# Optimization experiments

Measured on AMD Instinct MI355X. Metric: run time of the kernel, lower is better.

Reference implementation:

```python
import jax, jax.numpy as jnp
import numpy as np

NEG_SLOPE = 0.2  # PyG GATConv default negative_slope


def _gat_layer(x, src, dst, W, a_s, a_d, b, heads, ch):
    N = x.shape[0]
    h = (x @ W).reshape(N, heads, ch)                      # [N,H,C]
    al_s = jnp.sum(h * a_s[None], axis=-1)                 # [N,H]
    al_d = jnp.sum(h * a_d[None], axis=-1)                 # [N,H]
    e = jax.nn.leaky_relu(al_s[src] + al_d[dst], NEG_SLOPE)  # [E,H]
    m = jax.ops.segment_max(e, dst, num_segments=N)        # segment-softmax (stable)
    ex = jnp.exp(e - jax.lax.stop_gradient(m)[dst])
    denom = jax.ops.segment_sum(ex, dst, num_segments=N)
    alpha = ex / (denom[dst] + 1e-16)                      # [E,H]
    msg = h[src] * alpha[..., None]                        # [E,H,C]
    out = jax.ops.segment_sum(msg, dst, num_segments=N)    # [N,H,C]
    return out.reshape(N, heads * ch) + b


def _add_self_loops(edge_index, N):
    loop = jnp.arange(N, dtype=edge_index.dtype)
    src = jnp.concatenate([edge_index[0], loop])
    dst = jnp.concatenate([edge_index[1], loop])
    return src, dst


def gat_forward(x, edge_index, batch, W1, a_src1, a_dst1, b1, W2, a_src2, a_dst2, b2, W3, a_src3, a_dst3, b3, num_graphs=512):
    N = x.shape[0]
    src, dst = _add_self_loops(edge_index, N)
    x = jax.nn.relu(_gat_layer(x, src, dst, W1, a_src1, a_dst1, b1, 4, 64))
    x = jax.nn.relu(_gat_layer(x, src, dst, W2, a_src2, a_dst2, b2, 4, 64))
    x = _gat_layer(x, src, dst, W3, a_src3, a_dst3, b3, 1, 32)
    # global_mean_pool
    sums = jax.ops.segment_sum(x, batch, num_segments=num_graphs)
    cnt = jax.ops.segment_sum(jnp.ones((N,), x.dtype), batch, num_segments=num_graphs)
    return sums / jnp.maximum(cnt, 1.0)[:, None]


def setup_inputs() -> dict:
    key = jax.random.key(0)
    ks = jax.random.split(key, 16)
    N, E, G = 50000, 800000, 512
    IN, HID, H, OUT = 775, 64, 4, 32
    s = 0.05
    return {
        "x": jax.random.normal(ks[0], (N, IN), jnp.float32),
        "edge_index": jax.random.randint(ks[1], (2, E), 0, N, jnp.int32),
        "batch": jnp.sort(jax.random.randint(ks[2], (N,), 0, G, jnp.int32)),
        "W1": jax.random.normal(ks[3], (IN, H * HID), jnp.float32) * s,
        "a_src1": jax.random.normal(ks[4], (H, HID), jnp.float32) * s,
        "a_dst1": jax.random.normal(ks[5], (H, HID), jnp.float32) * s,
        "b1": jnp.zeros((H * HID,), jnp.float32),
        "W2": jax.random.normal(ks[6], (H * HID, H * HID), jnp.float32) * s,
        "a_src2": jax.random.normal(ks[7], (H, HID), jnp.float32) * s,
        "a_dst2": jax.random.normal(ks[8], (H, HID), jnp.float32) * s,
        "b2": jnp.zeros((H * HID,), jnp.float32),
        "W3": jax.random.normal(ks[9], (H * HID, OUT), jnp.float32) * s,
        "a_src3": jax.random.normal(ks[10], (1, OUT), jnp.float32) * s,
        "a_dst3": jax.random.normal(ks[11], (1, OUT), jnp.float32) * s,
        "b3": jnp.zeros((OUT,), jnp.float32),
    }


def reference(x, edge_index, batch, W1, a_src1, a_dst1, b1, W2, a_src2, a_dst2, b2, W3, a_src3, a_dst3, b3):
    return gat_forward(x, edge_index, batch, W1, a_src1, a_dst1, b1, W2, a_src2, a_dst2, b2, W3, a_src3, a_dst3, b3)
```

## Files before the change

kernel.cpp:

```cpp
#include <hip/hip_runtime.h>
#include <hip/hip_bf16.h>

typedef unsigned short u16;
typedef __attribute__((ext_vector_type(4))) unsigned short u16x4;
typedef __attribute__((ext_vector_type(8))) unsigned short u16x8;
typedef __attribute__((ext_vector_type(8))) short bf16x8;
typedef __attribute__((ext_vector_type(4))) float f32x4;

__device__ __forceinline__ u16 f2bs(float f) {
    union { float f; unsigned int u; } x; x.f = f;
    unsigned int r = x.u + 0x7FFFu + ((x.u >> 16) & 1u);
    return (u16)(r >> 16);
}
__device__ __forceinline__ float bs2f(u16 u) {
    union { unsigned int u; float f; } x; x.u = ((unsigned int)u) << 16; return x.f;
}
__device__ __forceinline__ float lrelu(float e) { return e >= 0.f ? e : 0.2f * e; }

__device__ __forceinline__ unsigned cvtpk(float lo, float hi) {
    unsigned r;
    asm("v_cvt_pk_bf16_f32 %0, %1, %2" : "=v"(r) : "v"(lo), "v"(hi));
    return r;
}

__device__ __forceinline__ void glds16(const void* g, void* l) {
    __builtin_amdgcn_global_load_lds(
        (const __attribute__((address_space(1))) unsigned int*)g,
        (__attribute__((address_space(3))) unsigned int*)l, 16, 0, 0);
}

__global__ void deg_kernel(const int* __restrict__ dst, int* __restrict__ deg, int E) {
    int i = blockIdx.x * 256 + threadIdx.x;
    if (i < E) atomicAdd(&deg[dst[i]], 1);
}

__global__ __launch_bounds__(1024) void scan_local(const int* __restrict__ deg,
        int* __restrict__ ptr, int* __restrict__ bsum, int N) {
    __shared__ int wsum[16];
    const int t = threadIdx.x, i = blockIdx.x * 1024 + t;
    const int lane = t & 63, w = t >> 6;
    int v = (i < N) ? deg[i] : 0;
    int x = v;
    #pragma unroll
    for (int off = 1; off < 64; off <<= 1) { int y = __shfl_up(x, off); if (lane >= off) x += y; }
    if (lane == 63) wsum[w] = x;
    __syncthreads();
    if (w == 0) {
        int s = (lane < 16) ? wsum[lane] : 0;
        #pragma unroll
        for (int off = 1; off < 16; off <<= 1) { int y = __shfl_up(s, off); if (lane >= off) s += y; }
        if (lane < 16) wsum[lane] = s;
    }
    __syncthreads();
    int incl = x + (w > 0 ? wsum[w - 1] : 0);
    if (i < N) ptr[i + 1] = incl;
    if (t == 0) bsum[blockIdx.x] = wsum[15];
}

__global__ __launch_bounds__(64) void scan_carry(int* __restrict__ bsum, int nb) {
    int t = threadIdx.x;
    int v = (t < nb) ? bsum[t] : 0;
    int x = v;
    #pragma unroll
    for (int off = 1; off < 64; off <<= 1) { int y = __shfl_up(x, off); if (t >= off) x += y; }
    if (t < nb) bsum[t] = x - v;
}

__global__ __launch_bounds__(1024) void scan_final(const int* __restrict__ deg,
        int* __restrict__ ptr, int* __restrict__ cur, const int* __restrict__ bsum, int N) {
    int i = blockIdx.x * 1024 + threadIdx.x;
    if (i == 0) ptr[0] = 0;
    if (i < N) {
        int p = ptr[i + 1] + bsum[blockIdx.x];
        ptr[i + 1] = p;
        cur[i] = p - deg[i];
    }
}

__global__ void fill_kernel(const int* __restrict__ src, const int* __restrict__ dst,
        int* __restrict__ cur, int* __restrict__ csr, int E) {
    int i = blockIdx.x * 256 + threadIdx.x;
    if (i < E) { int p = atomicAdd(&cur[dst[i]], 1); csr[p] = src[i]; }
}

__global__ void bounds_kernel(const int* __restrict__ batch, int* __restrict__ gstart,
        int N, int G) {
    int i = blockIdx.x * 256 + threadIdx.x;
    if (i > N) return;
    if (i == 0) {
        int b0 = batch[0];
        for (int g = 0; g <= b0; g++) gstart[g] = 0;
    } else if (i == N) {
        int bl = batch[N - 1];
        for (int g = bl + 1; g <= G; g++) gstart[g] = N;
    } else {
        int b = batch[i], bp = batch[i - 1];
        for (int g = bp + 1; g <= b; g++) gstart[g] = i;
    }
}

__global__ void transpose_w(const float* __restrict__ W, u16* __restrict__ Wt,
        int K, int Nn, int KT) {
    int idx = blockIdx.x * 256 + threadIdx.x;
    if (idx >= Nn * KT) return;
    int n = idx / KT, k = idx - n * KT;
    Wt[(size_t)n * KT + k] = (k < K) ? f2bs(W[(size_t)k * Nn + n]) : (u16)0;
}

__global__ __launch_bounds__(256) void tail_kernel(const float* __restrict__ x,
        float* __restrict__ xtail, int N) {
    int idx = blockIdx.x * 256 + threadIdx.x;
    if (idx >= N * 32) return;
    int n = idx >> 5, j = idx & 31;
    xtail[idx] = (768 + j < 775) ? x[(size_t)n * 775 + 768 + j] : 0.f;
}

__global__ __launch_bounds__(256) void gemm_glds_f32(
        const float* __restrict__ A, int lda, int M,
        const float* __restrict__ Atail,
        const u16* __restrict__ B, int ldb,
        u16* __restrict__ C, int ldc) {
    __shared__ float Aldsf[3][128][32];
    __shared__ u16   Blds[3][128][32];
    const int t = threadIdx.x;
    const int col0 = blockIdx.x * 128;
    const int row0 = blockIdx.y * 128;
    const int wid = t >> 6, lane = t & 63;
    const int wm = wid >> 1, wn = wid & 1;
    const int quad = lane >> 4, l16 = lane & 15;

    f32x4 acc[4][4];
    f32x4 z = {0.f, 0.f, 0.f, 0.f};
    #pragma unroll
    for (int i = 0; i < 4; i++)
        #pragma unroll
        for (int j = 0; j < 4; j++) acc[i][j] = z;

    const int trb = wid * 32 + (lane >> 2);
    const int arl = lane >> 3;
    const int asg = lane & 7;

    auto stage = [&](int buf, int kt) {
        const int k0 = kt << 5;
        #pragma unroll
        for (int c = 0; c < 2; c++) {
            const int tr = trb + c * 16;
            const int ks = ((lane & 3) ^ ((tr >> 1) & 3)) * 8;
            glds16(B + (size_t)(col0 + tr) * ldb + k0 + ks, &Blds[buf][wid * 32 + c * 16][0]);
        }
        #pragma unroll
        for (int c = 0; c < 4; c++) {
            const int rt = wid * 32 + c * 8 + arl;
            int gra = row0 + rt; if (gra > M - 1) gra = M - 1;
            const int sg = (asg ^ ((rt & 3) << 1)) * 4;
            const float* src = (kt < 24) ? (A + (size_t)gra * lda + k0 + sg)
                                         : (Atail + (size_t)gra * 32 + sg);
            glds16(src, &Aldsf[buf][wid * 32 + c * 8][0]);
        }
    };
    auto compute = [&](int buf) {
        bf16x8 af[4], bfr[4];
        #pragma unroll
        for (int it = 0; it < 4; it++) {
            const int r = wm * 64 + it * 16 + l16;
            const int go = ((2 * quad) ^ ((r & 3) << 1)) * 4;
            const f32x4 lo = *(const f32x4*)&Aldsf[buf][r][go];
            const f32x4 hi = *(const f32x4*)&Aldsf[buf][r][go + 4];
            union { unsigned u[4]; bf16x8 v; } uu;
            uu.u[0] = cvtpk(lo[0], lo[1]);
            uu.u[1] = cvtpk(lo[2], lo[3]);
            uu.u[2] = cvtpk(hi[0], hi[1]);
            uu.u[3] = cvtpk(hi[2], hi[3]);
            af[it] = uu.v;
        }
        #pragma unroll
        for (int jt = 0; jt < 4; jt++) {
            const int r = wn * 64 + jt * 16 + l16;
            bfr[jt] = *(const bf16x8*)&Blds[buf][r][(quad ^ ((r >> 1) & 3)) * 8];
        }
        #pragma unroll
        for (int it = 0; it < 4; it++)
            #pragma unroll
            for (int jt = 0; jt < 4; jt++)
                acc[it][jt] = __builtin_amdgcn_mfma_f32_16x16x32_bf16(af[it], bfr[jt], acc[it][jt], 0, 0, 0);
    };

    const int kTiles = 25;
    stage(0, 0);
    stage(1, 1);
    for (int kt = 0; kt < kTiles - 1; ++kt) {
        asm volatile("s_waitcnt vmcnt(6)" ::: "memory");
        __builtin_amdgcn_sched_barrier(0);
        __builtin_amdgcn_s_barrier();
        __builtin_amdgcn_sched_barrier(0);
        if (kt + 2 < kTiles) stage((kt + 2) % 3, kt + 2);
        compute(kt % 3);
    }
    asm volatile("s_waitcnt vmcnt(0)" ::: "memory");
    __builtin_amdgcn_sched_barrier(0);
    __builtin_amdgcn_s_barrier();
    __builtin_amdgcn_sched_barrier(0);
    compute((kTiles - 1) % 3);

    #pragma unroll
    for (int it = 0; it < 4; it++) {
        int gr0 = row0 + wm * 64 + it * 16 + quad * 4;
        #pragma unroll
        for (int jt = 0; jt < 4; jt++) {
            int gc = col0 + wn * 64 + jt * 16 + l16;
            #pragma unroll
            for (int r = 0; r < 4; r++) {
                int gr = gr0 + r;
                if (gr < M) C[(size_t)gr * ldc + gc] = f2bs(acc[it][jt][r]);
            }
        }
    }
}

__global__ __launch_bounds__(256) void gemm_glds(
        const u16* __restrict__ A, int lda, int M, int K,
        const u16* __restrict__ B, int ldb,
        u16* __restrict__ C, int ldc) {
    __shared__ u16 Alds[3][128][32];
    __shared__ u16 Blds[3][128][32];
    const int t = threadIdx.x;
    const int col0 = blockIdx.x * 128;
    const int row0 = blockIdx.y * 128;
    const int wid = t >> 6, lane = t & 63;
    const int wm = wid >> 1, wn = wid & 1;
    const int quad = lane >> 4, l16 = lane & 15;

    f32x4 acc[4][4];
    f32x4 z = {0.f, 0.f, 0.f, 0.f};
    #pragma unroll
    for (int i = 0; i < 4; i++)
        #pragma unroll
        for (int j = 0; j < 4; j++) acc[i][j] = z;

    const int trb = wid * 32 + (lane >> 2);

    auto stage = [&](int buf, int kt) {
        const int k0 = kt << 5;
        #pragma unroll
        for (int c = 0; c < 2; c++) {
            const int tr = trb + c * 16;
            const int ks = ((lane & 3) ^ ((tr >> 1) & 3)) * 8;
            int gra = row0 + tr; if (gra > M - 1) gra = M - 1;
            glds16(A + (size_t)gra * lda + k0 + ks, &Alds[buf][wid * 32 + c * 16][0]);
            glds16(B + (size_t)(col0 + tr) * ldb + k0 + ks, &Blds[buf][wid * 32 + c * 16][0]);
        }
    };
    auto compute = [&](int buf) {
        bf16x8 af[4], bfr[4];
        #pragma unroll
        for (int it = 0; it < 4; it++) {
            const int r = wm * 64 + it * 16 + l16;
            af[it] = *(const bf16x8*)&Alds[buf][r][(quad ^ ((r >> 1) & 3)) * 8];
        }
        #pragma unroll
        for (int jt = 0; jt < 4; jt++) {
            const int r = wn * 64 + jt * 16 + l16;
            bfr[jt] = *(const bf16x8*)&Blds[buf][r][(quad ^ ((r >> 1) & 3)) * 8];
        }
        #pragma unroll
        for (int it = 0; it < 4; it++)
            #pragma unroll
            for (int jt = 0; jt < 4; jt++)
                acc[it][jt] = __builtin_amdgcn_mfma_f32_16x16x32_bf16(af[it], bfr[jt], acc[it][jt], 0, 0, 0);
    };

    const int kTiles = K >> 5;
    stage(0, 0);
    stage(1, 1);
    for (int kt = 0; kt < kTiles - 1; ++kt) {
        asm volatile("s_waitcnt vmcnt(4)" ::: "memory");
        __builtin_amdgcn_sched_barrier(0);
        __builtin_amdgcn_s_barrier();
        __builtin_amdgcn_sched_barrier(0);
        if (kt + 2 < kTiles) stage((kt + 2) % 3, kt + 2);
        compute(kt % 3);
    }
    asm volatile("s_waitcnt vmcnt(0)" ::: "memory");
    __builtin_amdgcn_sched_barrier(0);
    __builtin_amdgcn_s_barrier();
    __builtin_amdgcn_sched_barrier(0);
    compute((kTiles - 1) % 3);

    #pragma unroll
    for (int it = 0; it < 4; it++) {
        int gr0 = row0 + wm * 64 + it * 16 + quad * 4;
        #pragma unroll
        for (int jt = 0; jt < 4; jt++) {
            int gc = col0 + wn * 64 + jt * 16 + l16;
            #pragma unroll
            for (int r = 0; r < 4; r++) {
                int gr = gr0 + r;
                if (gr < M) C[(size_t)gr * ldc + gc] = f2bs(acc[it][jt][r]);
            }
        }
    }
}

__global__ __launch_bounds__(256) void gemm32(
        const u16* __restrict__ A, int lda, int M, int K,
        const u16* __restrict__ B, int ldb, float* __restrict__ C) {
    __shared__ u16 Alds[128][40];
    __shared__ u16 Blds[32][40];
    const int t = threadIdx.x;
    const int row0 = blockIdx.x * 128;
    const int wid = t >> 6, lane = t & 63;
    const int quad = lane >> 4, l16 = lane & 15;
    f32x4 acc[2][2];
    f32x4 z = {0.f, 0.f, 0.f, 0.f};
    acc[0][0] = z; acc[0][1] = z; acc[1][0] = z; acc[1][1] = z;
    const int kTiles = K >> 5;
    for (int kt = 0; kt < kTiles; ++kt) {
        const int k0 = kt << 5;
        #pragma unroll
        for (int c = 0; c < 2; c++) {
            int ch = t + c * 256;
            int r = ch >> 2, cp = (ch & 3) * 8;
            int gr = row0 + r;
            u16x8 v = {0,0,0,0,0,0,0,0};
            if (gr < M) v = *(const u16x8*)(A + (size_t)gr * lda + k0 + cp);
            *(u16x8*)&Alds[r][cp] = v;
        }
        if (t < 128) {
            int r = t >> 2, cp = (t & 3) * 8;
            *(u16x8*)&Blds[r][cp] = *(const u16x8*)(B + (size_t)r * ldb + k0 + cp);
        }
        __syncthreads();
        bf16x8 af[2], bfr[2];
        #pragma unroll
        for (int it = 0; it < 2; it++) af[it] = *(const bf16x8*)&Alds[wid * 32 + it * 16 + l16][quad * 8];
        #pragma unroll
        for (int jt = 0; jt < 2; jt++) bfr[jt] = *(const bf16x8*)&Blds[jt * 16 + l16][quad * 8];
        #pragma unroll
        for (int it = 0; it < 2; it++)
            #pragma unroll
            for (int jt = 0; jt < 2; jt++)
                acc[it][jt] = __builtin_amdgcn_mfma_f32_16x16x32_bf16(af[it], bfr[jt], acc[it][jt], 0, 0, 0);
        __syncthreads();
    }
    #pragma unroll
    for (int it = 0; it < 2; it++) {
        int gr0 = row0 + wid * 32 + it * 16 + quad * 4;
        #pragma unroll
        for (int jt = 0; jt < 2; jt++) {
            int gc = jt * 16 + l16;
            #pragma unroll
            for (int r = 0; r < 4; r++) {
                int gr = gr0 + r;
                if (gr < M) C[(size_t)gr * 32 + gc] = acc[it][jt][r];
            }
        }
    }
}

__global__ __launch_bounds__(256) void al_kernel(const u16* __restrict__ h,
        const float* __restrict__ a_s, const float* __restrict__ a_d,
        float* __restrict__ als, float* __restrict__ ald, int N) {
    const int t = threadIdx.x, wid = t >> 6, lane = t & 63;
    const f32x4 as4 = *(const f32x4*)&a_s[lane * 4];
    const f32x4 ad4 = *(const f32x4*)&a_d[lane * 4];
    #pragma unroll
    for (int u = 0; u < 2; u++) {
        const int n = blockIdx.x * 8 + wid * 2 + u;
        if (n >= N) return;
        const u16x4 hv = *(const u16x4*)&h[(size_t)n * 256 + lane * 4];
        float ps = 0.f, pd = 0.f;
        #pragma unroll
        for (int c = 0; c < 4; c++) {
            const float f = bs2f(hv[c]);
            ps = fmaf(f, as4[c], ps);
            pd = fmaf(f, ad4[c], pd);
        }
        #pragma unroll
        for (int off = 8; off >= 1; off >>= 1) {
            ps += __shfl_xor(ps, off, 16);
            pd += __shfl_xor(pd, off, 16);
        }
        if ((lane & 15) == 0) {
            als[n * 4 + (lane >> 4)] = ps;
            ald[n * 4 + (lane >> 4)] = pd;
        }
    }
}

__global__ __launch_bounds__(256) void al3_kernel(const float* __restrict__ h3,
        const float* __restrict__ a_s, const float* __restrict__ a_d,
        float* __restrict__ als, float* __restrict__ ald, int N) {
    int t = threadIdx.x, wid = t >> 6, lane = t & 63;
    int c = lane & 31, half = lane >> 5;
    float as = a_s[c], ad = a_d[c];
    int n = blockIdx.x * 8 + wid * 2 + half;
    if (n >= N) return;
    float hv = h3[(size_t)n * 32 + c];
    float ps = hv * as, pd = hv * ad;
    for (int off = 16; off >= 1; off >>= 1) { ps += __shfl_down(ps, off, 32); pd += __shfl_down(pd, off, 32); }
    if (c == 0) { als[n] = ps; ald[n] = pd; }
}

__global__ __launch_bounds__(256) void agg_kernel(const u16* __restrict__ hbuf,
        const float* __restrict__ als, const float* __restrict__ ald,
        const int* __restrict__ ptr, const int* __restrict__ csr,
        const float* __restrict__ bias, u16* __restrict__ act, int N) {
    __shared__ float al_lds[4][64][4];
    __shared__ int   s_lds[4][64];
    const int t = threadIdx.x, wid = t >> 6, lane = t & 63;
    const int i = blockIdx.x * 4 + wid;
    if (i >= N) return;
    const int start = ptr[i], end = ptr[i + 1];
    const int deg = end - start;
    const int col8 = lane & 31;
    const int half = lane >> 5;
    const int head8 = col8 >> 3;

    const f32x4 aldv = *(const f32x4*)&ald[(size_t)i * 4];
    const f32x4 alsv = *(const f32x4*)&als[(size_t)i * 4];
    f32x4 eself;
    #pragma unroll
    for (int hh = 0; hh < 4; hh++) eself[hh] = lrelu(alsv[hh] + aldv[hh]);

    float acc[8];
    f32x4 mx, inv;

    if (deg <= 64) {
        int sreg = 0;
        f32x4 ev;
        #pragma unroll
        for (int hh = 0; hh < 4; hh++) ev[hh] = -1e30f;
        if (lane < deg) {
            sreg = csr[start + lane];
            const f32x4 a = *(const f32x4*)&als[(size_t)sreg * 4];
            #pragma unroll
            for (int hh = 0; hh < 4; hh++) ev[hh] = lrelu(a[hh] + aldv[hh]);
        }
        #pragma unroll
        for (int hh = 0; hh < 4; hh++) mx[hh] = fmaxf(eself[hh], ev[hh]);
        #pragma unroll
        for (int off = 32; off >= 1; off >>= 1) {
            #pragma unroll
            for (int hh = 0; hh < 4; hh++) mx[hh] = fmaxf(mx[hh], __shfl_xor(mx[hh], off));
        }
        f32x4 sm, av;
        #pragma unroll
        for (int hh = 0; hh < 4; hh++) {
            av[hh] = (lane < deg) ? expf(ev[hh] - mx[hh]) : 0.f;
            sm[hh] = av[hh] + ((lane == 0) ? expf(eself[hh] - mx[hh]) : 0.f);
        }
        #pragma unroll
        for (int off = 32; off >= 1; off >>= 1) {
            #pragma unroll
            for (int hh = 0; hh < 4; hh++) sm[hh] += __shfl_xor(sm[hh], off);
        }
        #pragma unroll
        for (int hh = 0; hh < 4; hh++) inv[hh] = 1.f / (sm[hh] + 1e-16f);
        #pragma unroll
        for (int hh = 0; hh < 4; hh++) av[hh] *= inv[hh];
        *(f32x4*)&al_lds[wid][lane][0] = av;
        s_lds[wid][lane] = sreg;

        const u16x8 hrs = *(const u16x8*)&hbuf[(size_t)i * 256 + col8 * 8];
        const float aself = expf(eself[head8] - mx[head8]) * inv[head8];
        #pragma unroll
        for (int c = 0; c < 8; c++) acc[c] = (half == 0) ? aself * bs2f(hrs[c]) : 0.f;

        int k = half;
        for (; k + 6 < deg; k += 8) {
            const int s0 = s_lds[wid][k],     s1 = s_lds[wid][k + 2];
            const int s2 = s_lds[wid][k + 4], s3 = s_lds[wid][k + 6];
            const float a0 = al_lds[wid][k][head8],     a1 = al_lds[wid][k + 2][head8];
            const float a2 = al_lds[wid][k + 4][head8], a3 = al_lds[wid][k + 6][head8];
            const u16x8 h0 = *(const u16x8*)&hbuf[(size_t)s0 * 256 + col8 * 8];
            const u16x8 h1 = *(const u16x8*)&hbuf[(size_t)s1 * 256 + col8 * 8];
            const u16x8 h2 = *(const u16x8*)&hbuf[(size_t)s2 * 256 + col8 * 8];
            const u16x8 h3v = *(const u16x8*)&hbuf[(size_t)s3 * 256 + col8 * 8];
            #pragma unroll
            for (int c = 0; c < 8; c++) {
                acc[c] = fmaf(a0, bs2f(h0[c]), acc[c]);
                acc[c] = fmaf(a1, bs2f(h1[c]), acc[c]);
                acc[c] = fmaf(a2, bs2f(h2[c]), acc[c]);
                acc[c] = fmaf(a3, bs2f(h3v[c]), acc[c]);
            }
        }
        for (; k < deg; k += 2) {
            const int s = s_lds[wid][k];
            const float a = al_lds[wid][k][head8];
            const u16x8 hr = *(const u16x8*)&hbuf[(size_t)s * 256 + col8 * 8];
            #pragma unroll
            for (int c = 0; c < 8; c++) acc[c] = fmaf(a, bs2f(hr[c]), acc[c]);
        }
    } else {
        mx = eself;
        for (int j = start + lane; j < end; j += 64) {
            int s = csr[j];
            const f32x4 a = *(const f32x4*)&als[(size_t)s * 4];
            #pragma unroll
            for (int hh = 0; hh < 4; hh++) mx[hh] = fmaxf(mx[hh], lrelu(a[hh] + aldv[hh]));
        }
        #pragma unroll
        for (int off = 32; off >= 1; off >>= 1) {
            #pragma unroll
            for (int hh = 0; hh < 4; hh++) mx[hh] = fmaxf(mx[hh], __shfl_xor(mx[hh], off));
        }
        f32x4 sm;
        #pragma unroll
        for (int hh = 0; hh < 4; hh++) sm[hh] = (lane == 0) ? expf(eself[hh] - mx[hh]) : 0.f;
        for (int j = start + lane; j < end; j += 64) {
            int s = csr[j];
            const f32x4 a = *(const f32x4*)&als[(size_t)s * 4];
            #pragma unroll
            for (int hh = 0; hh < 4; hh++) sm[hh] += expf(lrelu(a[hh] + aldv[hh]) - mx[hh]);
        }
        #pragma unroll
        for (int off = 32; off >= 1; off >>= 1) {
            #pragma unroll
            for (int hh = 0; hh < 4; hh++) sm[hh] += __shfl_xor(sm[hh], off);
        }
        #pragma unroll
        for (int hh = 0; hh < 4; hh++) inv[hh] = 1.f / (sm[hh] + 1e-16f);

        const u16x8 hrs = *(const u16x8*)&hbuf[(size_t)i * 256 + col8 * 8];
        const float aself = expf(eself[head8] - mx[head8]) * inv[head8];
        #pragma unroll
        for (int c = 0; c < 8; c++) acc[c] = (half == 0) ? aself * bs2f(hrs[c]) : 0.f;

        for (int base = start; base < end; base += 64) {
            const int n64 = min(64, end - base);
            const int j = base + lane;
            int sreg = 0;
            if (j < end) {
                sreg = csr[j];
                const f32x4 a = *(const f32x4*)&als[(size_t)sreg * 4];
                f32x4 alpha;
                #pragma unroll
                for (int hh = 0; hh < 4; hh++)
                    alpha[hh] = expf(lrelu(a[hh] + aldv[hh]) - mx[hh]) * inv[hh];
                *(f32x4*)&al_lds[wid][lane][0] = alpha;
            }
            s_lds[wid][lane] = sreg;
            for (int k = half; k < n64; k += 2) {
                const int s = s_lds[wid][k];
                const float a = al_lds[wid][k][head8];
                const u16x8 hr = *(const u16x8*)&hbuf[(size_t)s * 256 + col8 * 8];
                #pragma unroll
                for (int c = 0; c < 8; c++) acc[c] = fmaf(a, bs2f(hr[c]), acc[c]);
            }
        }
    }

    #pragma unroll
    for (int c = 0; c < 8; c++) acc[c] += __shfl_down(acc[c], 32);
    if (half == 0) {
        const f32x4 bv0 = *(const f32x4*)&bias[col8 * 8];
        const f32x4 bv1 = *(const f32x4*)&bias[col8 * 8 + 4];
        u16x8 o;
        #pragma unroll
        for (int c = 0; c < 4; c++) o[c] = f2bs(fmaxf(acc[c] + bv0[c], 0.f));
        #pragma unroll
        for (int c = 4; c < 8; c++) o[c] = f2bs(fmaxf(acc[c] + bv1[c - 4], 0.f));
        *(u16x8*)&act[(size_t)i * 256 + col8 * 8] = o;
    }
}

__global__ __launch_bounds__(256) void agg3_kernel(const float* __restrict__ h3,
        const float* __restrict__ als, const float* __restrict__ ald,
        const int* __restrict__ ptr, const int* __restrict__ csr,
        const float* __restrict__ bias, float* __restrict__ out_n, int N) {
    __shared__ float a_lds[4][64];
    __shared__ int   s_lds3[4][64];
    const int t = threadIdx.x, wid = t >> 6, lane = t & 63;
    const int col = lane & 31, half = lane >> 5;
    const int i = blockIdx.x * 4 + wid;
    if (i >= N) return;
    const int start = ptr[i], end = ptr[i + 1];
    const int deg = end - start;
    const float aldv = ald[i];
    const float e0 = lrelu(als[i] + aldv);
    float acc = 0.f;

    if (deg <= 64) {
        int sreg = 0; float ev = -1e30f;
        if (lane < deg) { sreg = csr[start + lane]; ev = lrelu(als[sreg] + aldv); }
        float mx = fmaxf(e0, ev);
        #pragma unroll
        for (int off = 32; off >= 1; off >>= 1) mx = fmaxf(mx, __shfl_xor(mx, off));
        float ex = (lane < deg) ? expf(ev - mx) : 0.f;
        float sm = ex + ((lane == 0) ? expf(e0 - mx) : 0.f);
        #pragma unroll
        for (int off = 32; off >= 1; off >>= 1) sm += __shfl_xor(sm, off);
        const float inv = 1.f / (sm + 1e-16f);
        a_lds[wid][lane] = ex * inv;
        s_lds3[wid][lane] = sreg;
        if (half == 0) acc = expf(e0 - mx) * inv * h3[(size_t)i * 32 + col];

        int k = half;
        for (; k + 6 < deg; k += 8) {
            const int s0 = s_lds3[wid][k],     s1 = s_lds3[wid][k + 2];
            const int s2 = s_lds3[wid][k + 4], s3 = s_lds3[wid][k + 6];
            const float a0 = a_lds[wid][k],     a1 = a_lds[wid][k + 2];
            const float a2 = a_lds[wid][k + 4], a3 = a_lds[wid][k + 6];
            const float v0 = h3[(size_t)s0 * 32 + col];
            const float v1 = h3[(size_t)s1 * 32 + col];
            const float v2 = h3[(size_t)s2 * 32 + col];
            const float v3 = h3[(size_t)s3 * 32 + col];
            acc = fmaf(a0, v0, acc); acc = fmaf(a1, v1, acc);
            acc = fmaf(a2, v2, acc); acc = fmaf(a3, v3, acc);
        }
        for (; k < deg; k += 2)
            acc = fmaf(a_lds[wid][k], h3[(size_t)s_lds3[wid][k] * 32 + col], acc);
    } else {
        float mx = e0;
        for (int j = start + lane; j < end; j += 64)
            mx = fmaxf(mx, lrelu(als[csr[j]] + aldv));
        #pragma unroll
        for (int off = 32; off >= 1; off >>= 1) mx = fmaxf(mx, __shfl_xor(mx, off));
        float sm = (lane == 0) ? expf(e0 - mx) : 0.f;
        for (int j = start + lane; j < end; j += 64)
            sm += expf(lrelu(als[csr[j]] + aldv) - mx);
        #pragma unroll
        for (int off = 32; off >= 1; off >>= 1) sm += __shfl_xor(sm, off);
        const float inv = 1.f / (sm + 1e-16f);
        if (half == 0) acc = expf(e0 - mx) * inv * h3[(size_t)i * 32 + col];
        for (int base = start; base < end; base += 64) {
            const int n64 = min(64, end - base);
            const int j = base + lane;
            int sreg = 0; float av = 0.f;
            if (j < end) {
                sreg = csr[j];
                av = expf(lrelu(als[sreg] + aldv) - mx) * inv;
            }
            a_lds[wid][lane] = av;
            s_lds3[wid][lane] = sreg;
            for (int k = half; k < n64; k += 2)
                acc = fmaf(a_lds[wid][k], h3[(size_t)s_lds3[wid][k] * 32 + col], acc);
        }
    }

    acc += __shfl_down(acc, 32);
    if (half == 0)
        out_n[(size_t)i * 32 + col] = acc + bias[col];
}

__global__ __launch_bounds__(256) void pool_kernel(const float* __restrict__ out_n,
        const int* __restrict__ gstart, float* __restrict__ out, int G) {
    const int t = threadIdx.x, wid = t >> 6, lane = t & 63;
    const int col = lane & 31, half = lane >> 5;
    const int g = blockIdx.x * 4 + wid;
    if (g >= G) return;
    const int s = gstart[g], e = gstart[g + 1];
    float acc = 0.f;
    int r = s + half;
    for (; r + 6 < e; r += 8) {
        acc += out_n[(size_t)r * 32 + col];
        acc += out_n[(size_t)(r + 2) * 32 + col];
        acc += out_n[(size_t)(r + 4) * 32 + col];
        acc += out_n[(size_t)(r + 6) * 32 + col];
    }
    for (; r < e; r += 2) acc += out_n[(size_t)r * 32 + col];
    acc += __shfl_down(acc, 32);
    if (half == 0)
        out[g * 32 + col] = acc / fmaxf((float)(e - s), 1.f);
}

extern "C" void kernel_launch(void* const* d_in, const int* in_sizes, int n_in,
                              void* d_out, int out_size, void* d_ws, size_t ws_size,
                              hipStream_t stream) {
    const int N = 50000, E = 800000, G = 512;
    const float* x    = (const float*)d_in[0];
    const int*   ei   = (const int*)d_in[1];
    const int*   batch= (const int*)d_in[2];
    const float* W1   = (const float*)d_in[3];
    const float* as1  = (const float*)d_in[4];
    const float* ad1  = (const float*)d_in[5];
    const float* b1   = (const float*)d_in[6];
    const float* W2   = (const float*)d_in[7];
    const float* as2  = (const float*)d_in[8];
    const float* ad2  = (const float*)d_in[9];
    const float* b2   = (const float*)d_in[10];
    const float* W3   = (const float*)d_in[11];
    const float* as3  = (const float*)d_in[12];
    const float* ad3  = (const float*)d_in[13];
    const float* b3   = (const float*)d_in[14];
    const int* esrc = ei;
    const int* edst = ei + E;

    char* base = (char*)d_ws; size_t off = 0;
    auto alloc = [&](size_t bytes) -> void* {
        void* p = base + off; off = (off + bytes + 255) & ~(size_t)255; return p;
    };
    u16*   hbuf = (u16*)  alloc((size_t)N * 256 * 2);
    u16*   act  = (u16*)  alloc((size_t)N * 256 * 2);
    float* h3   = (float*)alloc((size_t)N * 32 * 4);
    float* als  = (float*)alloc((size_t)N * 4 * 4);
    float* ald  = (float*)alloc((size_t)N * 4 * 4);
    int*   deg  = (int*)  alloc((size_t)N * 4);
    int*   ptr  = (int*)  alloc((size_t)(N + 1) * 4);
    int*   cur  = (int*)  alloc((size_t)N * 4);
    int*   csr  = (int*)  alloc((size_t)E * 4);
    u16*   Wt   = (u16*)  alloc((size_t)256 * 800 * 2);
    int*   bsum = (int*)  alloc((size_t)64 * 4);
    float* out_n= (float*)alloc((size_t)N * 32 * 4);
    int*   gstart=(int*)  alloc((size_t)(G + 1) * 4);
    float* xtail= (float*)alloc((size_t)N * 32 * 4);

    hipMemsetAsync(deg, 0, (size_t)N * 4, stream);

    const int nb = (N + 1023) / 1024;
    deg_kernel<<<(E + 255) / 256, 256, 0, stream>>>(edst, deg, E);
    scan_local<<<nb, 1024, 0, stream>>>(deg, ptr, bsum, N);
    scan_carry<<<1, 64, 0, stream>>>(bsum, nb);
    scan_final<<<nb, 1024, 0, stream>>>(deg, ptr, cur, bsum, N);
    fill_kernel<<<(E + 255) / 256, 256, 0, stream>>>(esrc, edst, cur, csr, E);
    bounds_kernel<<<(N + 256) / 256, 256, 0, stream>>>(batch, gstart, N, G);

    dim3 gemmGrid(2, (N + 127) / 128);
    const int aggGrid = (N + 3) / 4;
    transpose_w<<<(256 * 800 + 255) / 256, 256, 0, stream>>>(W1, Wt, 775, 256, 800);
    tail_kernel<<<(N * 32 + 255) / 256, 256, 0, stream>>>(x, xtail, N);
    gemm_glds_f32<<<gemmGrid, 256, 0, stream>>>(x, 775, N, xtail, Wt, 800, hbuf, 256);
    al_kernel<<<(N + 7) / 8, 256, 0, stream>>>(hbuf, as1, ad1, als, ald, N);
    agg_kernel<<<aggGrid, 256, 0, stream>>>(hbuf, als, ald, ptr, csr, b1, act, N);
    transpose_w<<<(256 * 256 + 255) / 256, 256, 0, stream>>>(W2, Wt, 256, 256, 256);
    gemm_glds<<<gemmGrid, 256, 0, stream>>>(act, 256, N, 256, Wt, 256, hbuf, 256);
    al_kernel<<<(N + 7) / 8, 256, 0, stream>>>(hbuf, as2, ad2, als, ald, N);
    agg_kernel<<<aggGrid, 256, 0, stream>>>(hbuf, als, ald, ptr, csr, b2, act, N);
    transpose_w<<<(32 * 256 + 255) / 256, 256, 0, stream>>>(W3, Wt, 256, 32, 256);
    gemm32<<<(N + 127) / 128, 256, 0, stream>>>(act, 256, N, 256, Wt, 256, h3);
    al3_kernel<<<(N + 7) / 8, 256, 0, stream>>>(h3, as3, ad3, als, ald, N);
    agg3_kernel<<<aggGrid, 256, 0, stream>>>(h3, als, ald, ptr, csr, b3, out_n, N);
    pool_kernel<<<(G + 3) / 4, 256, 0, stream>>>(out_n, gstart, (float*)d_out, G);
}
```

Before: 617.3 us.

## Fuse attention logit computation into GEMM epilogues and swizzle blocks across XCDs

The per-node source and destination attention logits for layers 1 and 2 are now computed in the GEMM epilogue from the bf16-rounded accumulators, using a 16-lane shuffle reduction per head. This removes the separate al_kernel launches and their re-read of the hidden buffer. The GEMM grid is flattened to 1D and remapped so that consecutive tiles land on the same XCD, which is meant to improve L2 reuse. The MFMA block is also wrapped in s_setprio raises. The epilogue now loops rows in the outer position, which changes its store pattern and adds shuffle work inside the GEMM.

```diff
diff --git a/kernel.cpp b/kernel.cpp
--- a/kernel.cpp
+++ b/kernel.cpp
@@ -27,6 +27,13 @@
     __builtin_amdgcn_global_load_lds(
         (const __attribute__((address_space(1))) unsigned int*)g,
         (__attribute__((address_space(3))) unsigned int*)l, 16, 0, 0);
+}
+
+__device__ __forceinline__ int xcd_swz(int bid, int nwg) {
+    int q = nwg >> 3, r = nwg & 7;
+    int xcd = bid & 7, pos = bid >> 3;
+    int base = (xcd < r) ? xcd * (q + 1) : r * (q + 1) + (xcd - r) * q;
+    return base + pos;
 }
 
 __global__ void deg_kernel(const int* __restrict__ dst, int* __restrict__ deg, int E) {
@@ -119,12 +126,16 @@
         const float* __restrict__ A, int lda, int M,
         const float* __restrict__ Atail,
         const u16* __restrict__ B, int ldb,
-        u16* __restrict__ C, int ldc) {
+        u16* __restrict__ C, int ldc,
+        const float* __restrict__ a_s, const float* __restrict__ a_d,
+        float* __restrict__ als, float* __restrict__ ald) {
     __shared__ float Aldsf[3][128][32];
     __shared__ u16   Blds[3][128][32];
     const int t = threadIdx.x;
-    const int col0 = blockIdx.x * 128;
-    const int row0 = blockIdx.y * 128;
+    const int id = xcd_swz(blockIdx.x, gridDim.x);
+    const int cx = id & 1;
+    const int col0 = cx * 128;
+    const int row0 = (id >> 1) * 128;
     const int wid = t >> 6, lane = t & 63;
     const int wm = wid >> 1, wn = wid & 1;
     const int quad = lane >> 4, l16 = lane & 15;
@@ -178,11 +189,13 @@
             const int r = wn * 64 + jt * 16 + l16;
             bfr[jt] = *(const bf16x8*)&Blds[buf][r][(quad ^ ((r >> 1) & 3)) * 8];
         }
+        __builtin_amdgcn_s_setprio(1);
         #pragma unroll
         for (int it = 0; it < 4; it++)
             #pragma unroll
             for (int jt = 0; jt < 4; jt++)
                 acc[it][jt] = __builtin_amdgcn_mfma_f32_16x16x32_bf16(af[it], bfr[jt], acc[it][jt], 0, 0, 0);
+        __builtin_amdgcn_s_setprio(0);
     };
 
     const int kTiles = 25;
@@ -202,16 +215,42 @@
     __builtin_amdgcn_sched_barrier(0);
     compute((kTiles - 1) % 3);
 
+    const int hd = cx * 2 + wn;
+    float asv[4], adv[4];
+    #pragma unroll
+    for (int jt = 0; jt < 4; jt++) {
+        asv[jt] = a_s[hd * 64 + jt * 16 + l16];
+        adv[jt] = a_d[hd * 64 + jt * 16 + l16];
+    }
     #pragma unroll
     for (int it = 0; it < 4; it++) {
         int gr0 = row0 + wm * 64 + it * 16 + quad * 4;
         #pragma unroll
-        for (int jt = 0; jt < 4; jt++) {
-            int gc = col0 + wn * 64 + jt * 16 + l16;
-            #pragma unroll
-            for (int r = 0; r < 4; r++) {
-                int gr = gr0 + r;
-                if (gr < M) C[(size_t)gr * ldc + gc] = f2bs(acc[it][jt][r]);
+        for (int r = 0; r < 4; r++) {
+            int gr = gr0 + r;
+            u16 ov[4];
+            float ps = 0.f, pd = 0.f;
+            #pragma unroll
+            for (int jt = 0; jt < 4; jt++) {
+                u16 o = f2bs(acc[it][jt][r]);
+                ov[jt] = o;
+                float hv = bs2f(o);
+                ps = fmaf(hv, asv[jt], ps);
+                pd = fmaf(hv, adv[jt], pd);
+            }
+            if (gr < M) {
+                #pragma unroll
+                for (int jt = 0; jt < 4; jt++)
+                    C[(size_t)gr * ldc + col0 + wn * 64 + jt * 16 + l16] = ov[jt];
+            }
+            #pragma unroll
+            for (int off = 8; off >= 1; off >>= 1) {
+                ps += __shfl_xor(ps, off, 16);
+                pd += __shfl_xor(pd, off, 16);
+            }
+            if (l16 == 0 && gr < M) {
+                als[gr * 4 + hd] = ps;
+                ald[gr * 4 + hd] = pd;
             }
         }
     }
@@ -220,12 +259,16 @@
 __global__ __launch_bounds__(256) void gemm_glds(
         const u16* __restrict__ A, int lda, int M, int K,
         const u16* __restrict__ B, int ldb,
-        u16* __restrict__ C, int ldc) {
+        u16* __restrict__ C, int ldc,
+        const float* __restrict__ a_s, const float* __restrict__ a_d,
+        float* __restrict__ als, float* __restrict__ ald) {
     __shared__ u16 Alds[3][128][32];
     __shared__ u16 Blds[3][128][32];
     const int t = threadIdx.x;
-    const int col0 = blockIdx.x * 128;
-    const int row0 = blockIdx.y * 128;
+    const int id = xcd_swz(blockIdx.x, gridDim.x);
+    const int cx = id & 1;
+    const int col0 = cx * 128;
+    const int row0 = (id >> 1) * 128;
     const int wid = t >> 6, lane = t & 63;
     const int wm = wid >> 1, wn = wid & 1;
     const int quad = lane >> 4, l16 = lane & 15;
@@ -262,11 +305,13 @@
             const int r = wn * 64 + jt * 16 + l16;
             bfr[jt] = *(const bf16x8*)&Blds[buf][r][(quad ^ ((r >> 1) & 3)) * 8];
         }
+        __builtin_amdgcn_s_setprio(1);
         #pragma unroll
         for (int it = 0; it < 4; it++)
             #pragma unroll
             for (int jt = 0; jt < 4; jt++)
                 acc[it][jt] = __builtin_amdgcn_mfma_f32_16x16x32_bf16(af[it], bfr[jt], acc[it][jt], 0, 0, 0);
+        __builtin_amdgcn_s_setprio(0);
     };
 
     const int kTiles = K >> 5;
@@ -286,16 +331,42 @@
     __builtin_amdgcn_sched_barrier(0);
     compute((kTiles - 1) % 3);
 
+    const int hd = cx * 2 + wn;
+    float asv[4], adv[4];
+    #pragma unroll
+    for (int jt = 0; jt < 4; jt++) {
+        asv[jt] = a_s[hd * 64 + jt * 16 + l16];
+        adv[jt] = a_d[hd * 64 + jt * 16 + l16];
+    }
     #pragma unroll
     for (int it = 0; it < 4; it++) {
         int gr0 = row0 + wm * 64 + it * 16 + quad * 4;
         #pragma unroll
-        for (int jt = 0; jt < 4; jt++) {
-            int gc = col0 + wn * 64 + jt * 16 + l16;
-            #pragma unroll
-            for (int r = 0; r < 4; r++) {
-                int gr = gr0 + r;
-                if (gr < M) C[(size_t)gr * ldc + gc] = f2bs(acc[it][jt][r]);
+        for (int r = 0; r < 4; r++) {
+            int gr = gr0 + r;
+            u16 ov[4];
+            float ps = 0.f, pd = 0.f;
+            #pragma unroll
+            for (int jt = 0; jt < 4; jt++) {
+                u16 o = f2bs(acc[it][jt][r]);
+                ov[jt] = o;
+                float hv = bs2f(o);
+                ps = fmaf(hv, asv[jt], ps);
+                pd = fmaf(hv, adv[jt], pd);
+            }
+            if (gr < M) {
+                #pragma unroll
+                for (int jt = 0; jt < 4; jt++)
+                    C[(size_t)gr * ldc + col0 + wn * 64 + jt * 16 + l16] = ov[jt];
+            }
+            #pragma unroll
+            for (int off = 8; off >= 1; off >>= 1) {
+                ps += __shfl_xor(ps, off, 16);
+                pd += __shfl_xor(pd, off, 16);
+            }
+            if (l16 == 0 && gr < M) {
+                als[gr * 4 + hd] = ps;
+                ald[gr * 4 + hd] = pd;
             }
         }
     }
@@ -353,36 +424,6 @@
                 int gr = gr0 + r;
                 if (gr < M) C[(size_t)gr * 32 + gc] = acc[it][jt][r];
             }
-        }
-    }
-}
-
-__global__ __launch_bounds__(256) void al_kernel(const u16* __restrict__ h,
-        const float* __restrict__ a_s, const float* __restrict__ a_d,
-        float* __restrict__ als, float* __restrict__ ald, int N) {
-    const int t = threadIdx.x, wid = t >> 6, lane = t & 63;
-    const f32x4 as4 = *(const f32x4*)&a_s[lane * 4];
-    const f32x4 ad4 = *(const f32x4*)&a_d[lane * 4];
-    #pragma unroll
-    for (int u = 0; u < 2; u++) {
-        const int n = blockIdx.x * 8 + wid * 2 + u;
-        if (n >= N) return;
-        const u16x4 hv = *(const u16x4*)&h[(size_t)n * 256 + lane * 4];
-        float ps = 0.f, pd = 0.f;
-        #pragma unroll
-        for (int c = 0; c < 4; c++) {
-            const float f = bs2f(hv[c]);
-            ps = fmaf(f, as4[c], ps);
-            pd = fmaf(f, ad4[c], pd);
-        }
-        #pragma unroll
-        for (int off = 8; off >= 1; off >>= 1) {
-            ps += __shfl_xor(ps, off, 16);
-            pd += __shfl_xor(pd, off, 16);
-        }
-        if ((lane & 15) == 0) {
-            als[n * 4 + (lane >> 4)] = ps;
-            ald[n * 4 + (lane >> 4)] = pd;
         }
     }
 }
@@ -715,16 +756,16 @@
     fill_kernel<<<(E + 255) / 256, 256, 0, stream>>>(esrc, edst, cur, csr, E);
     bounds_kernel<<<(N + 256) / 256, 256, 0, stream>>>(batch, gstart, N, G);
 
-    dim3 gemmGrid(2, (N + 127) / 128);
+    const int gemmGrid = 2 * ((N + 127) / 128);
     const int aggGrid = (N + 3) / 4;
     transpose_w<<<(256 * 800 + 255) / 256, 256, 0, stream>>>(W1, Wt, 775, 256, 800);
     tail_kernel<<<(N * 32 + 255) / 256, 256, 0, stream>>>(x, xtail, N);
-    gemm_glds_f32<<<gemmGrid, 256, 0, stream>>>(x, 775, N, xtail, Wt, 800, hbuf, 256);
-    al_kernel<<<(N + 7) / 8, 256, 0, stream>>>(hbuf, as1, ad1, als, ald, N);
+    gemm_glds_f32<<<gemmGrid, 256, 0, stream>>>(x, 775, N, xtail, Wt, 800, hbuf, 256,
+                                                as1, ad1, als, ald);
     agg_kernel<<<aggGrid, 256, 0, stream>>>(hbuf, als, ald, ptr, csr, b1, act, N);
     transpose_w<<<(256 * 256 + 255) / 256, 256, 0, stream>>>(W2, Wt, 256, 256, 256);
-    gemm_glds<<<gemmGrid, 256, 0, stream>>>(act, 256, N, 256, Wt, 256, hbuf, 256);
-    al_kernel<<<(N + 7) / 8, 256, 0, stream>>>(hbuf, as2, ad2, als, ald, N);
+    gemm_glds<<<gemmGrid, 256, 0, stream>>>(act, 256, N, 256, Wt, 256, hbuf, 256,
+                                            as2, ad2, als, ald);
     agg_kernel<<<aggGrid, 256, 0, stream>>>(hbuf, als, ald, ptr, csr, b2, act, N);
     transpose_w<<<(32 * 256 + 255) / 256, 256, 0, stream>>>(W3, Wt, 256, 32, 256);
     gemm32<<<(N + 127) / 128, 256, 0, stream>>>(act, 256, N, 256, Wt, 256, h3);
```

Result: no change. 611.3 us (median of 2 runs) (-1.0%).
